# Optimization experiments

Measured on AMD Instinct MI355X. Metric: run time of the kernel, lower is better.

Reference implementation:

```python
import jax, jax.numpy as jnp
import numpy as np

VOCAB, D, TYPES = 100000, 128, 128
T, B = 409600, 8192

def setup_inputs() -> dict:
    key = jax.random.key(0)
    k1, k2, k3, k4 = jax.random.split(key, 4)
    feature_seq = jax.random.randint(k1, (T,), 0, VOCAB, dtype=jnp.int64 if jax.config.read('jax_enable_x64') else jnp.int32)
    offset_seq = jnp.sort(jax.random.randint(k2, (B,), 0, T, dtype=feature_seq.dtype))
    offset_seq = offset_seq.at[0].set(0)  # torch EmbeddingBag requires offsets[0] == 0
    W = jax.random.normal(k3, (VOCAB, D), dtype=jnp.float32) * 0.1
    L = jax.random.normal(k4, (TYPES, 2 * D), dtype=jnp.float32) * 0.05
    return {"feature_seq": feature_seq, "offset_seq": offset_seq, "W": W, "L": L}

def reference(feature_seq, offset_seq, W, L):
    n_tok = feature_seq.shape[0]
    n_bag = offset_seq.shape[0]
    # map each token position to its bag id (offsets are sorted bag starts)
    seg = jnp.searchsorted(offset_seq, jnp.arange(n_tok), side='right') - 1  # [T]
    emb = W[feature_seq]                                                     # [T, D] gather
    counts = jax.ops.segment_sum(jnp.ones((n_tok,), W.dtype), seg, num_segments=n_bag)  # [B]
    ssum = jax.ops.segment_sum(emb, seg, num_segments=n_bag)                 # [B, D]
    mean = ssum / jnp.maximum(counts, 1.0)[:, None]
    smax = jax.ops.segment_max(emb, seg, num_segments=n_bag)                 # [B, D]
    smax = jnp.where(counts[:, None] > 0, smax, 0.0)                         # empty bags -> 0
    men = jnp.concatenate([mean, smax], axis=-1)                             # [B, 2D]
    # dropout is identity in eval mode; linear has no bias
    return men @ L.T                                                         # [B, TYPES]
```

## Files before the change

### kernel.cpp

```cpp
#include <hip/hip_runtime.h>
#include <cfloat>


constexpr int D     = 128;
constexpr int TYPES = 128;
constexpr int BPB   = 4;

__global__ __launch_bounds__(256, 8)
void embbag_men_linear(const int* __restrict__ feat,
                       const int* __restrict__ offs,
                       const float* __restrict__ W,
                       const float* __restrict__ L,
                       float* __restrict__ out,
                       int T, int B)
{
    __shared__ float4 men[BPB][64];
    __shared__ float  partial[BPB][TYPES];

    const int tid  = threadIdx.x;
    const int wv   = tid >> 6;
    const int lane = tid & 63;
    const int slot = lane >> 5;
    const int g    = lane & 31;
    const int bag0 = blockIdx.x * BPB;
    const int bag  = bag0 + wv;

    int start = 0, end = 0;
    if (bag < B) {
        start = offs[bag];
        end   = (bag + 1 < B) ? offs[bag + 1] : T;
    }

    float4 s4 = make_float4(0.f, 0.f, 0.f, 0.f);
    float4 m4 = make_float4(-FLT_MAX, -FLT_MAX, -FLT_MAX, -FLT_MAX);

    const float* __restrict__ Wg = W + 4 * g;

    int i = start + slot;
    for (; i + 6 < end; i += 8) {
        const int i0 = feat[i];
        const int i1 = feat[i + 2];
        const int i2 = feat[i + 4];
        const int i3 = feat[i + 6];
        const float4 v0 = *reinterpret_cast<const float4*>(Wg + (size_t)i0 * D);
        const float4 v1 = *reinterpret_cast<const float4*>(Wg + (size_t)i1 * D);
        const float4 v2 = *reinterpret_cast<const float4*>(Wg + (size_t)i2 * D);
        const float4 v3 = *reinterpret_cast<const float4*>(Wg + (size_t)i3 * D);
        s4.x += v0.x + v1.x + v2.x + v3.x;
        s4.y += v0.y + v1.y + v2.y + v3.y;
        s4.z += v0.z + v1.z + v2.z + v3.z;
        s4.w += v0.w + v1.w + v2.w + v3.w;
        m4.x = fmaxf(fmaxf(fmaxf(m4.x, v0.x), fmaxf(v1.x, v2.x)), v3.x);
        m4.y = fmaxf(fmaxf(fmaxf(m4.y, v0.y), fmaxf(v1.y, v2.y)), v3.y);
        m4.z = fmaxf(fmaxf(fmaxf(m4.z, v0.z), fmaxf(v1.z, v2.z)), v3.z);
        m4.w = fmaxf(fmaxf(fmaxf(m4.w, v0.w), fmaxf(v1.w, v2.w)), v3.w);
    }
    for (; i < end; i += 2) {
        const int idx = feat[i];
        const float4 v = *reinterpret_cast<const float4*>(Wg + (size_t)idx * D);
        s4.x += v.x; s4.y += v.y; s4.z += v.z; s4.w += v.w;
        m4.x = fmaxf(m4.x, v.x); m4.y = fmaxf(m4.y, v.y);
        m4.z = fmaxf(m4.z, v.z); m4.w = fmaxf(m4.w, v.w);
    }

    s4.x += __shfl_xor(s4.x, 32); s4.y += __shfl_xor(s4.y, 32);
    s4.z += __shfl_xor(s4.z, 32); s4.w += __shfl_xor(s4.w, 32);
    m4.x = fmaxf(m4.x, __shfl_xor(m4.x, 32));
    m4.y = fmaxf(m4.y, __shfl_xor(m4.y, 32));
    m4.z = fmaxf(m4.z, __shfl_xor(m4.z, 32));
    m4.w = fmaxf(m4.w, __shfl_xor(m4.w, 32));

    if (lane < 32) {
        const int  n     = end - start;
        const bool empty = (n <= 0);
        const float inv  = 1.0f / (float)(empty ? 1 : n);
        men[wv][g]      = make_float4(s4.x * inv, s4.y * inv,
                                      s4.z * inv, s4.w * inv);
        men[wv][32 + g] = empty ? make_float4(0.f, 0.f, 0.f, 0.f) : m4;
    }
    __syncthreads();

    const int o = tid & (TYPES - 1);
    const int h = tid >> 7;

    float acc[BPB];
    #pragma unroll
    for (int b = 0; b < BPB; ++b) acc[b] = 0.f;

    const float* Lrow = L + (size_t)o * (2 * D) + h * D;
    #pragma unroll 8
    for (int k4 = 0; k4 < D / 4; ++k4) {
        const float4 lv = *reinterpret_cast<const float4*>(Lrow + 4 * k4);
        #pragma unroll
        for (int b = 0; b < BPB; ++b) {
            const float4 mv = men[b][h * 32 + k4];
            acc[b] = fmaf(lv.x, mv.x, acc[b]);
            acc[b] = fmaf(lv.y, mv.y, acc[b]);
            acc[b] = fmaf(lv.z, mv.z, acc[b]);
            acc[b] = fmaf(lv.w, mv.w, acc[b]);
        }
    }

    if (h == 1) {
        #pragma unroll
        for (int b = 0; b < BPB; ++b) partial[b][o] = acc[b];
    }
    __syncthreads();
    if (h == 0) {
        #pragma unroll
        for (int b = 0; b < BPB; ++b) {
            const int bg = bag0 + b;
            if (bg < B)
                out[(size_t)bg * TYPES + o] = acc[b] + partial[b][o];
        }
    }
}

extern "C" void kernel_launch(void* const* d_in, const int* in_sizes, int n_in,
                              void* d_out, int out_size, void* d_ws, size_t ws_size,
                              hipStream_t stream)
{
    const int*   feat = (const int*)d_in[0];
    const int*   offs = (const int*)d_in[1];
    const float* W    = (const float*)d_in[2];
    const float* L    = (const float*)d_in[3];
    float*       out  = (float*)d_out;

    const int T = in_sizes[0];
    const int B = in_sizes[1];
    const int grid = (B + BPB - 1) / BPB;
    embbag_men_linear<<<grid, 256, 0, stream>>>(feat, offs, W, L, out, T, B);
}
```

Measured before the change: 75.04 us.

## Use two waves per bag with contiguous quarter splits and 8-deep gather unroll

```diff
diff --git a/kernel.cpp b/kernel.cpp
--- a/kernel.cpp
+++ b/kernel.cpp
@@ -5,8 +5,10 @@
 constexpr int D     = 128;
 constexpr int TYPES = 128;
 constexpr int BPB   = 4;
+constexpr int WPB   = 2;
+constexpr int BLOCK = 512;
 
-__global__ __launch_bounds__(256, 8)
+__global__ __launch_bounds__(BLOCK, 8)
 void embbag_men_linear(const int* __restrict__ feat,
                        const int* __restrict__ offs,
                        const float* __restrict__ W,
@@ -15,47 +17,51 @@
                        int T, int B)
 {
     __shared__ float4 men[BPB][64];
-    __shared__ float  partial[BPB][TYPES];
+    __shared__ float4 redS[BPB][WPB][32];
+    __shared__ float4 redM[BPB][WPB][32];
+    __shared__ float  partial[3][BPB][TYPES];
 
     const int tid  = threadIdx.x;
     const int wv   = tid >> 6;
     const int lane = tid & 63;
+    const int bi   = wv >> 1;
+    const int wh   = wv & 1;
     const int slot = lane >> 5;
     const int g    = lane & 31;
     const int bag0 = blockIdx.x * BPB;
-    const int bag  = bag0 + wv;
+    const int bag  = bag0 + bi;
 
     int start = 0, end = 0;
     if (bag < B) {
         start = offs[bag];
         end   = (bag + 1 < B) ? offs[bag + 1] : T;
     }
+    const int n  = end - start;
+    const int q  = wh * 2 + slot;
+    const int qa = start + (n * q) / 4;
+    const int qb = start + (n * (q + 1)) / 4;
 
     float4 s4 = make_float4(0.f, 0.f, 0.f, 0.f);
     float4 m4 = make_float4(-FLT_MAX, -FLT_MAX, -FLT_MAX, -FLT_MAX);
-
     const float* __restrict__ Wg = W + 4 * g;
 
-    int i = start + slot;
-    for (; i + 6 < end; i += 8) {
-        const int i0 = feat[i];
-        const int i1 = feat[i + 2];
-        const int i2 = feat[i + 4];
-        const int i3 = feat[i + 6];
-        const float4 v0 = *reinterpret_cast<const float4*>(Wg + (size_t)i0 * D);
-        const float4 v1 = *reinterpret_cast<const float4*>(Wg + (size_t)i1 * D);
-        const float4 v2 = *reinterpret_cast<const float4*>(Wg + (size_t)i2 * D);
-        const float4 v3 = *reinterpret_cast<const float4*>(Wg + (size_t)i3 * D);
-        s4.x += v0.x + v1.x + v2.x + v3.x;
-        s4.y += v0.y + v1.y + v2.y + v3.y;
-        s4.z += v0.z + v1.z + v2.z + v3.z;
-        s4.w += v0.w + v1.w + v2.w + v3.w;
-        m4.x = fmaxf(fmaxf(fmaxf(m4.x, v0.x), fmaxf(v1.x, v2.x)), v3.x);
-        m4.y = fmaxf(fmaxf(fmaxf(m4.y, v0.y), fmaxf(v1.y, v2.y)), v3.y);
-        m4.z = fmaxf(fmaxf(fmaxf(m4.z, v0.z), fmaxf(v1.z, v2.z)), v3.z);
-        m4.w = fmaxf(fmaxf(fmaxf(m4.w, v0.w), fmaxf(v1.w, v2.w)), v3.w);
+    int i = qa;
+    for (; i + 8 <= qb; i += 8) {
+        int idx[8];
+        #pragma unroll
+        for (int j = 0; j < 8; ++j) idx[j] = feat[i + j];
+        float4 v[8];
+        #pragma unroll
+        for (int j = 0; j < 8; ++j)
+            v[j] = *reinterpret_cast<const float4*>(Wg + (size_t)idx[j] * D);
+        #pragma unroll
+        for (int j = 0; j < 8; ++j) {
+            s4.x += v[j].x; s4.y += v[j].y; s4.z += v[j].z; s4.w += v[j].w;
+            m4.x = fmaxf(m4.x, v[j].x); m4.y = fmaxf(m4.y, v[j].y);
+            m4.z = fmaxf(m4.z, v[j].z); m4.w = fmaxf(m4.w, v[j].w);
+        }
     }
-    for (; i < end; i += 2) {
+    for (; i < qb; ++i) {
         const int idx = feat[i];
         const float4 v = *reinterpret_cast<const float4*>(Wg + (size_t)idx * D);
         s4.x += v.x; s4.y += v.y; s4.z += v.z; s4.w += v.w;
@@ -71,12 +77,22 @@
     m4.w = fmaxf(m4.w, __shfl_xor(m4.w, 32));
 
     if (lane < 32) {
-        const int  n     = end - start;
-        const bool empty = (n <= 0);
-        const float inv  = 1.0f / (float)(empty ? 1 : n);
-        men[wv][g]      = make_float4(s4.x * inv, s4.y * inv,
-                                      s4.z * inv, s4.w * inv);
-        men[wv][32 + g] = empty ? make_float4(0.f, 0.f, 0.f, 0.f) : m4;
+        redS[bi][wh][g] = s4;
+        redM[bi][wh][g] = m4;
+    }
+    __syncthreads();
+
+    if (wh == 0 && lane < 32) {
+        const float4 a0 = redS[bi][0][g], a1 = redS[bi][1][g];
+        const float4 b0 = redM[bi][0][g], b1 = redM[bi][1][g];
+        const bool  empty = (n <= 0);
+        const float inv   = 1.0f / (float)(empty ? 1 : n);
+        men[bi][g] = make_float4((a0.x + a1.x) * inv, (a0.y + a1.y) * inv,
+                                 (a0.z + a1.z) * inv, (a0.w + a1.w) * inv);
+        men[bi][32 + g] = empty
+            ? make_float4(0.f, 0.f, 0.f, 0.f)
+            : make_float4(fmaxf(b0.x, b1.x), fmaxf(b0.y, b1.y),
+                          fmaxf(b0.z, b1.z), fmaxf(b0.w, b1.w));
     }
     __syncthreads();
 
@@ -87,13 +103,13 @@
     #pragma unroll
     for (int b = 0; b < BPB; ++b) acc[b] = 0.f;
 
-    const float* Lrow = L + (size_t)o * (2 * D) + h * D;
-    #pragma unroll 8
-    for (int k4 = 0; k4 < D / 4; ++k4) {
+    const float* Lrow = L + (size_t)o * (2 * D) + h * 64;
+    #pragma unroll
+    for (int k4 = 0; k4 < 16; ++k4) {
         const float4 lv = *reinterpret_cast<const float4*>(Lrow + 4 * k4);
         #pragma unroll
         for (int b = 0; b < BPB; ++b) {
-            const float4 mv = men[b][h * 32 + k4];
+            const float4 mv = men[b][h * 16 + k4];
             acc[b] = fmaf(lv.x, mv.x, acc[b]);
             acc[b] = fmaf(lv.y, mv.y, acc[b]);
             acc[b] = fmaf(lv.z, mv.z, acc[b]);
@@ -101,9 +117,9 @@
         }
     }
 
-    if (h == 1) {
+    if (h > 0) {
         #pragma unroll
-        for (int b = 0; b < BPB; ++b) partial[b][o] = acc[b];
+        for (int b = 0; b < BPB; ++b) partial[h - 1][b][o] = acc[b];
     }
     __syncthreads();
     if (h == 0) {
@@ -111,7 +127,8 @@
         for (int b = 0; b < BPB; ++b) {
             const int bg = bag0 + b;
             if (bg < B)
-                out[(size_t)bg * TYPES + o] = acc[b] + partial[b][o];
+                out[(size_t)bg * TYPES + o] =
+                    acc[b] + partial[0][b][o] + partial[1][b][o] + partial[2][b][o];
         }
     }
 }
@@ -129,5 +146,5 @@
     const int T = in_sizes[0];
     const int B = in_sizes[1];
     const int grid = (B + BPB - 1) / BPB;
-    embbag_men_linear<<<grid, 256, 0, stream>>>(feat, offs, W, L, out, T, B);
+    embbag_men_linear<<<grid, BLOCK, 0, stream>>>(feat, offs, W, L, out, T, B);
 }
```

After: 67.06 us. 1.12x faster.
